# Kernel optimization log

Measured on AMD Instinct MI355X. Metric: run time of the kernel, lower is better.

Reference implementation:

```python
import jax, jax.numpy as jnp
import numpy as np


def setup_inputs() -> dict:
    key = jax.random.key(0)
    k1, k2, k3, k4 = jax.random.split(key, 4)
    B, D, F = 524288, 64, 32
    stdv = 1.0 / np.sqrt(D)
    x = jax.random.normal(k1, (B, D), dtype=jnp.float32)
    us = jax.random.uniform(k2, (F, D), dtype=jnp.float32, minval=-stdv, maxval=stdv)
    ws = jax.random.uniform(k3, (F, D), dtype=jnp.float32, minval=-stdv, maxval=stdv)
    bs = jax.random.uniform(k4, (F,), dtype=jnp.float32, minval=-0.01, maxval=0.01)
    return {"x": x, "us": us, "ws": ws, "bs": bs}


def _planar_step(carry, params):
    z, sum_log_det = carry
    u, w, b = params  # u,w: [D], b: scalar
    # constrained u for invertibility: u_hat = u + (softplus(wu) - 1 - wu) * w / ||w||
    wu = jnp.dot(u, w)
    u_hat = u + (jax.nn.softplus(wu) - 1.0 - wu) * w / jnp.linalg.norm(w)
    lin = z @ w + b                      # [B]
    h = jnp.tanh(lin)                    # [B]
    z_new = z + u_hat[None, :] * h[:, None]
    h_prime = 1.0 - h * h                # [B]
    # psi @ u_hat = h'(lin) * (w . u_hat)
    log_det = jnp.log(jnp.abs(1.0 + h_prime * jnp.dot(w, u_hat)))
    return (z_new, sum_log_det + log_det), None


def reference(x, us, ws, bs):
    init = (x, jnp.zeros(x.shape[0], dtype=x.dtype))
    (z, sum_log_det), _ = jax.lax.scan(_planar_step, init, (us, ws, bs))
    return z, sum_log_det
```

## Files before the change

### kernel.cpp

```cpp
#include <hip/hip_runtime.h>
#include <math.h>


#define NF_D 64
#define NF_F 32

typedef float f4 __attribute__((ext_vector_type(4)));
typedef float f32x4v __attribute__((ext_vector_type(4)));
typedef unsigned int u32;
typedef u32 u32x4 __attribute__((ext_vector_type(4)));
typedef short bf16x8 __attribute__((ext_vector_type(8)));

#define WS_WF   0
#define WS_UF   2048
#define WS_GT   3072
#define WS_WUH  4096
#define WS_TOT  4128

__device__ __forceinline__ u32 fbits(float x){ union{float f;u32 u;} c; c.f=x; return c.u; }
__device__ __forceinline__ float asf(u32 u){ union{u32 u;float f;} c; c.u=u; return c.f; }
__device__ __forceinline__ u32 bfrnd(float x){ u32 b=fbits(x); return (b + 0x7FFFu + ((b>>16)&1u)) >> 16; }
__device__ __forceinline__ bf16x8 asbf(u32x4 v){ union{u32x4 u; bf16x8 b;} c; c.u=v; return c.b; }

__global__ void nf_precompute(const float* __restrict__ us,
                              const float* __restrict__ ws,
                              u32* __restrict__ wsb) {
  __shared__ float s_u[NF_F][NF_D];
  float* wsf = (float*)wsb;
  int t = threadIdx.x;
  if (t < NF_F) {
    const float* u = us + t * NF_D;
    const float* w = ws + t * NF_D;
    float wu = 0.f, n2 = 0.f;
    for (int d = 0; d < NF_D; ++d) {
      wu = fmaf(u[d], w[d], wu);
      n2 = fmaf(w[d], w[d], n2);
    }
    float sp = fmaxf(wu, 0.f) + log1pf(expf(-fabsf(wu)));
    float coef = (sp - 1.f - wu) / sqrtf(n2);
    for (int d = 0; d < NF_D; ++d)
      s_u[t][d] = fmaf(coef, w[d], u[d]);
    wsf[WS_WUH + t] = fmaf(coef, n2, wu);
  }
  __syncthreads();
  for (int idx = t; idx < 8 * 64; idx += 256) {
    int lin = idx >> 6, l = idx & 63;
    int Mt = lin >> 2, Kt = (lin >> 1) & 1, p = lin & 1;
    int fm = 16 * Mt + (l & 15);
    int kb = 32 * Kt + 8 * (l >> 4);
    for (int i = 0; i < 4; ++i) {
      u32 pr[2];
      for (int e = 0; e < 2; ++e) {
        float w = ws[fm * NF_D + kb + 2 * i + e];
        u32 hb = fbits(w) & 0xFFFF0000u;
        pr[e] = (p == 0) ? (hb >> 16) : (fbits(w - asf(hb)) >> 16);
      }
      wsb[WS_WF + (lin * 64 + l) * 4 + i] = pr[0] | (pr[1] << 16);
    }
  }
  for (int idx = t; idx < 4 * 64; idx += 256) {
    int l = idx & 63;
    int d = 16 * (idx >> 6) + (l & 15);
    int fb = 8 * (l >> 4);
    for (int i = 0; i < 4; ++i) {
      u32 r0 = bfrnd(s_u[fb + 2 * i][d]);
      u32 r1 = bfrnd(s_u[fb + 2 * i + 1][d]);
      wsb[WS_UF + idx * 4 + i] = r0 | (r1 << 16);
    }
  }
  for (int i = t; i < NF_F * NF_F; i += 256) {
    int f = i >> 5, g = i & 31;
    float s = 0.f;
    if (g < f) {
      const float* w = ws + f * NF_D;
      for (int d = 0; d < NF_D; ++d) s = fmaf(s_u[g][d], w[d], s);
    }
    wsf[WS_GT + i] = s;
  }
}

__device__ __forceinline__ float fast_tanh(float x) {
  float e = __builtin_amdgcn_exp2f(x * 2.885390081777927f);
  return 1.f - 2.f * __builtin_amdgcn_rcpf(e + 1.f);
}

#define MFMA __builtin_amdgcn_mfma_f32_16x16x32_bf16

__global__ __launch_bounds__(256) void nf_main(
    const float* __restrict__ x,
    const float* __restrict__ bs,
    const u32* __restrict__ wsb,
    float* __restrict__ out_z,
    float* __restrict__ out_ld,
    int B) {
  __shared__ float S[4][64 * 33];
  const float* wsf = (const float*)wsb;

  int wave = threadIdx.x >> 6;
  int l = threadIdx.x & 63;
  int ntiles = B / 64;
  int tile = blockIdx.x * 4 + wave;
  if (tile >= ntiles) tile = ntiles - 1;
  float* Sw = S[wave];

  bf16x8 Wf[2][2][2], Uf[4];
  #pragma unroll
  for (int q = 0; q < 8; ++q)
    Wf[q >> 2][(q >> 1) & 1][q & 1] =
        asbf(*(const u32x4*)(wsb + WS_WF + (q * 64 + l) * 4));
  #pragma unroll
  for (int Nt = 0; Nt < 4; ++Nt)
    Uf[Nt] = asbf(*(const u32x4*)(wsb + WS_UF + (Nt * 64 + l) * 4));

  const float* xt = x + (size_t)tile * 64 * NF_D;

  #pragma unroll
  for (int Nt = 0; Nt < 4; ++Nt) {
    bf16x8 Xh[2], Xl[2];
    #pragma unroll
    for (int Kt = 0; Kt < 2; ++Kt) {
      const f4* xp = (const f4*)(xt + ((l & 15) + 16 * Nt) * NF_D +
                                 32 * Kt + 8 * (l >> 4));
      f4 xa = xp[0], xb = xp[1];
      float xs[8] = {xa.x, xa.y, xa.z, xa.w, xb.x, xb.y, xb.z, xb.w};
      u32x4 hw, lw;
      #pragma unroll
      for (int i = 0; i < 4; ++i) {
        u32 b0 = fbits(xs[2 * i]), b1 = fbits(xs[2 * i + 1]);
        u32 h0 = b0 & 0xFFFF0000u, h1 = b1 & 0xFFFF0000u;
        hw[i] = (h0 >> 16) | h1;
        lw[i] = (fbits(xs[2 * i] - asf(h0)) >> 16) |
                (fbits(xs[2 * i + 1] - asf(h1)) & 0xFFFF0000u);
      }
      Xh[Kt] = asbf(hw);
      Xl[Kt] = asbf(lw);
    }
    #pragma unroll
    for (int Mt = 0; Mt < 2; ++Mt) {
      f32x4v a = {0.f, 0.f, 0.f, 0.f};
      #pragma unroll
      for (int Kt = 0; Kt < 2; ++Kt) {
        a = MFMA(Wf[Mt][Kt][0], Xh[Kt], a, 0, 0, 0);
        a = MFMA(Wf[Mt][Kt][0], Xl[Kt], a, 0, 0, 0);
        a = MFMA(Wf[Mt][Kt][1], Xh[Kt], a, 0, 0, 0);
      }
      #pragma unroll
      for (int r = 0; r < 4; ++r)
        Sw[((l & 15) + 16 * Nt) * 33 + 16 * Mt + 4 * (l >> 4) + r] = a[r];
    }
  }

  const float* gt = wsf + WS_GT;
  const float* wuhp = wsf + WS_WUH;
  f4 hq[8];
  #pragma unroll
  for (int q = 0; q < 8; ++q) hq[q] = (f4)(0.f);
  float ldp = 1.f;
  #pragma unroll
  for (int f = 0; f < NF_F; ++f) {
    const f4* g4 = (const f4*)(gt + f * 32);
    f4 a = (f4)(0.f);
    #pragma unroll
    for (int q = 0; q < (f + 3) / 4; ++q)
      a += g4[q] * hq[q];
    float s = Sw[l * 33 + f] + bs[f] + ((a.x + a.y) + (a.z + a.w));
    float hf = fast_tanh(s);
    ldp *= fmaf(fmaf(-hf, hf, 1.f), wuhp[f], 1.f);
    hq[f >> 2][f & 3] = hf;
  }
  #pragma unroll
  for (int i = 0; i < 16; ++i) {
    u32 pk = (fbits(hq[i >> 1][(i & 1) * 2]) >> 16) |
             (fbits(hq[i >> 1][(i & 1) * 2 + 1]) & 0xFFFF0000u);
    Sw[i * 64 + l] = asf(pk);
  }

  bf16x8 Hf[4];
  #pragma unroll
  for (int Mt = 0; Mt < 4; ++Mt) {
    u32x4 hw;
    #pragma unroll
    for (int i = 0; i < 4; ++i)
      hw[i] = fbits(Sw[(4 * (l >> 4) + i) * 64 + (l & 15) + 16 * Mt]);
    Hf[Mt] = asbf(hw);
  }

  float* zt = out_z + (size_t)tile * 64 * NF_D;
  #pragma unroll
  for (int Mt = 0; Mt < 4; ++Mt) {
    #pragma unroll
    for (int Nt = 0; Nt < 4; ++Nt) {
      f32x4v zz = {0.f, 0.f, 0.f, 0.f};
      zz = MFMA(Hf[Mt], Uf[Nt], zz, 0, 0, 0);
      #pragma unroll
      for (int r = 0; r < 4; ++r) {
        int brow = 16 * Mt + 4 * (l >> 4) + r;
        int d = (l & 15) + 16 * Nt;
        zt[brow * NF_D + d] = zz[r] + xt[brow * NF_D + d];
      }
    }
  }
  out_ld[(size_t)tile * 64 + l] =
      __builtin_amdgcn_logf(fabsf(ldp)) * 0.6931471805599453f;
}

extern "C" void kernel_launch(void* const* d_in, const int* in_sizes, int n_in,
                              void* d_out, int out_size, void* d_ws, size_t ws_size,
                              hipStream_t stream) {
  const float* x    = (const float*)d_in[0];
  const float* us   = (const float*)d_in[1];
  const float* ws_p = (const float*)d_in[2];
  const float* bs   = (const float*)d_in[3];
  const int B = in_sizes[0] / NF_D;

  u32* wsbuf = (u32*)d_ws;
  float* out = (float*)d_out;

  nf_precompute<<<1, 256, 0, stream>>>(us, ws_p, wsbuf);
  const int ntiles = B / 64;
  const int grid = (ntiles + 3) / 4;
  nf_main<<<grid, 256, 0, stream>>>(x, bs, wsbuf, out,
                                    out + (size_t)B * NF_D, B);
}
```

Measured before the change: 81.03 us.

## Use forward-accumulating triangular update and transposed MFMA for vectorized z stores

Result: slower. 93.64 us (+15.6%).

```diff
diff --git a/kernel.cpp b/kernel.cpp
--- a/kernel.cpp
+++ b/kernel.cpp
@@ -71,9 +71,9 @@
   for (int i = t; i < NF_F * NF_F; i += 256) {
     int f = i >> 5, g = i & 31;
     float s = 0.f;
-    if (g < f) {
-      const float* w = ws + f * NF_D;
-      for (int d = 0; d < NF_D; ++d) s = fmaf(s_u[g][d], w[d], s);
+    if (g > f) {
+      const float* w = ws + g * NF_D;
+      for (int d = 0; d < NF_D; ++d) s = fmaf(s_u[f][d], w[d], s);
     }
     wsf[WS_GT + i] = s;
   }
@@ -150,54 +150,57 @@
     }
   }
 
-  const float* gt = wsf + WS_GT;
+  const float* gc = wsf + WS_GT;
   const float* wuhp = wsf + WS_WUH;
-  f4 hq[8];
-  #pragma unroll
-  for (int q = 0; q < 8; ++q) hq[q] = (f4)(0.f);
+  const f4* bs4 = (const f4*)bs;
+  f4 sa[8];
+  #pragma unroll
+  for (int q = 0; q < 8; ++q) {
+    f4 sv;
+    #pragma unroll
+    for (int e = 0; e < 4; ++e) sv[e] = Sw[l * 33 + 4 * q + e];
+    sa[q] = sv + bs4[q];
+  }
   float ldp = 1.f;
   #pragma unroll
   for (int f = 0; f < NF_F; ++f) {
-    const f4* g4 = (const f4*)(gt + f * 32);
-    f4 a = (f4)(0.f);
-    #pragma unroll
-    for (int q = 0; q < (f + 3) / 4; ++q)
-      a += g4[q] * hq[q];
-    float s = Sw[l * 33 + f] + bs[f] + ((a.x + a.y) + (a.z + a.w));
-    float hf = fast_tanh(s);
+    float hf = fast_tanh(sa[f >> 2][f & 3]);
     ldp *= fmaf(fmaf(-hf, hf, 1.f), wuhp[f], 1.f);
-    hq[f >> 2][f & 3] = hf;
+    const f4* gr = (const f4*)(gc + f * 32);
+    #pragma unroll
+    for (int q = f >> 2; q < 8; ++q)
+      sa[q] += gr[q] * hf;
+    sa[f >> 2][f & 3] = hf;
   }
   #pragma unroll
   for (int i = 0; i < 16; ++i) {
-    u32 pk = (fbits(hq[i >> 1][(i & 1) * 2]) >> 16) |
-             (fbits(hq[i >> 1][(i & 1) * 2 + 1]) & 0xFFFF0000u);
+    u32 pk = (fbits(sa[i >> 1][(i & 1) * 2]) >> 16) |
+             (fbits(sa[i >> 1][(i & 1) * 2 + 1]) & 0xFFFF0000u);
     Sw[i * 64 + l] = asf(pk);
   }
 
   bf16x8 Hf[4];
   #pragma unroll
-  for (int Mt = 0; Mt < 4; ++Mt) {
+  for (int Nt = 0; Nt < 4; ++Nt) {
     u32x4 hw;
     #pragma unroll
     for (int i = 0; i < 4; ++i)
-      hw[i] = fbits(Sw[(4 * (l >> 4) + i) * 64 + (l & 15) + 16 * Mt]);
-    Hf[Mt] = asbf(hw);
+      hw[i] = fbits(Sw[(4 * (l >> 4) + i) * 64 + (l & 15) + 16 * Nt]);
+    Hf[Nt] = asbf(hw);
   }
 
   float* zt = out_z + (size_t)tile * 64 * NF_D;
   #pragma unroll
-  for (int Mt = 0; Mt < 4; ++Mt) {
-    #pragma unroll
-    for (int Nt = 0; Nt < 4; ++Nt) {
+  for (int Ntb = 0; Ntb < 4; ++Ntb) {
+    #pragma unroll
+    for (int Mtd = 0; Mtd < 4; ++Mtd) {
       f32x4v zz = {0.f, 0.f, 0.f, 0.f};
-      zz = MFMA(Hf[Mt], Uf[Nt], zz, 0, 0, 0);
-      #pragma unroll
-      for (int r = 0; r < 4; ++r) {
-        int brow = 16 * Mt + 4 * (l >> 4) + r;
-        int d = (l & 15) + 16 * Nt;
-        zt[brow * NF_D + d] = zz[r] + xt[brow * NF_D + d];
-      }
+      zz = MFMA(Uf[Mtd], Hf[Ntb], zz, 0, 0, 0);
+      int b = (l & 15) + 16 * Ntb;
+      int d0 = 16 * Mtd + 4 * (l >> 4);
+      f4 xr = *(const f4*)(xt + b * NF_D + d0);
+      f4 zv = {zz[0] + xr.x, zz[1] + xr.y, zz[2] + xr.z, zz[3] + xr.w};
+      *(f4*)(zt + b * NF_D + d0) = zv;
     }
   }
   out_ld[(size_t)tile * 64 + l] =
```

## Transpose output MFMA for vectorized z stores and XOR-swizzle LDS tile

Applied to the files above, without the earlier changes.

Measured after the change: 85.87 us. 6.0% more time.

```diff
diff --git a/kernel.cpp b/kernel.cpp
--- a/kernel.cpp
+++ b/kernel.cpp
@@ -93,7 +93,7 @@
     float* __restrict__ out_z,
     float* __restrict__ out_ld,
     int B) {
-  __shared__ float S[4][64 * 33];
+  __shared__ float S[4][2048];
   const float* wsf = (const float*)wsb;
 
   int wave = threadIdx.x >> 6;
@@ -144,9 +144,11 @@
         a = MFMA(Wf[Mt][Kt][0], Xl[Kt], a, 0, 0, 0);
         a = MFMA(Wf[Mt][Kt][1], Xh[Kt], a, 0, 0, 0);
       }
+      int b = (l & 15) + 16 * Nt;
+      int fc = 16 * Mt + 4 * (l >> 4);
       #pragma unroll
       for (int r = 0; r < 4; ++r)
-        Sw[((l & 15) + 16 * Nt) * 33 + 16 * Mt + 4 * (l >> 4) + r] = a[r];
+        Sw[b * 32 + ((fc + r) ^ (b & 31))] = a[r];
     }
   }
 
@@ -163,7 +165,8 @@
     #pragma unroll
     for (int q = 0; q < (f + 3) / 4; ++q)
       a += g4[q] * hq[q];
-    float s = Sw[l * 33 + f] + bs[f] + ((a.x + a.y) + (a.z + a.w));
+    float s = Sw[l * 32 + (f ^ (l & 31))] + bs[f] +
+              ((a.x + a.y) + (a.z + a.w));
     float hf = fast_tanh(s);
     ldp *= fmaf(fmaf(-hf, hf, 1.f), wuhp[f], 1.f);
     hq[f >> 2][f & 3] = hf;
@@ -177,27 +180,26 @@
 
   bf16x8 Hf[4];
   #pragma unroll
-  for (int Mt = 0; Mt < 4; ++Mt) {
+  for (int Nt = 0; Nt < 4; ++Nt) {
     u32x4 hw;
     #pragma unroll
     for (int i = 0; i < 4; ++i)
-      hw[i] = fbits(Sw[(4 * (l >> 4) + i) * 64 + (l & 15) + 16 * Mt]);
-    Hf[Mt] = asbf(hw);
+      hw[i] = fbits(Sw[(4 * (l >> 4) + i) * 64 + (l & 15) + 16 * Nt]);
+    Hf[Nt] = asbf(hw);
   }
 
   float* zt = out_z + (size_t)tile * 64 * NF_D;
   #pragma unroll
-  for (int Mt = 0; Mt < 4; ++Mt) {
-    #pragma unroll
-    for (int Nt = 0; Nt < 4; ++Nt) {
+  for (int Ntb = 0; Ntb < 4; ++Ntb) {
+    #pragma unroll
+    for (int Mtd = 0; Mtd < 4; ++Mtd) {
       f32x4v zz = {0.f, 0.f, 0.f, 0.f};
-      zz = MFMA(Hf[Mt], Uf[Nt], zz, 0, 0, 0);
-      #pragma unroll
-      for (int r = 0; r < 4; ++r) {
-        int brow = 16 * Mt + 4 * (l >> 4) + r;
-        int d = (l & 15) + 16 * Nt;
-        zt[brow * NF_D + d] = zz[r] + xt[brow * NF_D + d];
-      }
+      zz = MFMA(Uf[Mtd], Hf[Ntb], zz, 0, 0, 0);
+      int b = (l & 15) + 16 * Ntb;
+      int d0 = 16 * Mtd + 4 * (l >> 4);
+      f4 xr = *(const f4*)(xt + b * NF_D + d0);
+      f4 zv = {zz[0] + xr.x, zz[1] + xr.y, zz[2] + xr.z, zz[3] + xr.w};
+      *(f4*)(zt + b * NF_D + d0) = zv;
     }
   }
   out_ld[(size_t)tile * 64 + l] =
```
